# Performance work log

Hardware: AMD Instinct MI355X
Metric: run time of the kernel (lower is better)

Reference implementation:

```python
import jax, jax.numpy as jnp
import numpy as np

K_NEIGH = 12
RADIUS = 0.5


def _mlp(x, w1, b1, w2, b2):
    return jax.nn.relu(x @ w1 + b1) @ w2 + b2


def _angle(a, b):
    # atan2(||a x b||, a.b), as in PyG point-pair features
    c = jnp.cross(a, b)
    return jnp.arctan2(jnp.linalg.norm(c, axis=-1), jnp.sum(a * b, axis=-1))


def _quat_to_mat(q):
    w, x, y, z = q[:, 0], q[:, 1], q[:, 2], q[:, 3]
    m = jnp.stack([
        1 - 2 * (y * y + z * z), 2 * (x * y - z * w), 2 * (x * z + y * w),
        2 * (x * y + z * w), 1 - 2 * (x * x + z * z), 2 * (y * z - x * w),
        2 * (x * z - y * w), 2 * (y * z + x * w), 1 - 2 * (x * x + y * y),
    ], axis=-1)
    return m.reshape(-1, 3, 3)


def _lin_params(key, fan_in, fan_out):
    kw, kb = jax.random.split(key)
    s = 1.0 / np.sqrt(fan_in)
    w = jax.random.uniform(kw, (fan_in, fan_out), minval=-s, maxval=s, dtype=jnp.float32)
    b = jax.random.uniform(kb, (fan_out,), minval=-s, maxval=s, dtype=jnp.float32)
    return w, b


def setup_inputs() -> dict:
    key = jax.random.key(0)
    keys = jax.random.split(key, 8)
    points = jax.random.uniform(keys[0], (1, 128, 64, 3), dtype=jnp.float32)
    dims = [(7, 32, 16), (19, 32, 8), (24, 32, 16), (16, 32, 8), (24, 32, 16), (16, 32, 12), (27, 64, 1)]
    names = ['l1', 'g1', 'l2', 'g2', 'l3', 'g3', 'l4']
    inp = {'points': points}
    for i, (nm, (di, dh, do)) in enumerate(zip(names, dims)):
        k1, k2 = jax.random.split(keys[i + 1])
        w1, b1 = _lin_params(k1, di, dh)
        w2, b2 = _lin_params(k2, dh, do)
        inp[nm + '_w1'], inp[nm + '_b1'], inp[nm + '_w2'], inp[nm + '_b2'] = w1, b1, w2, b2
    return inp


def reference(points, l1_w1, l1_b1, l1_w2, l1_b2, g1_w1, g1_b1, g1_w2, g1_b2,
              l2_w1, l2_b1, l2_w2, l2_b2, g2_w1, g2_b1, g2_w2, g2_b2,
              l3_w1, l3_b1, l3_w2, l3_b2, g3_w1, g3_b1, g3_w2, g3_b2,
              l4_w1, l4_b1, l4_w2, l4_b2):
    B, H, W, _ = points.shape
    pos = points.reshape(-1, 3)          # [N,3]
    N = pos.shape[0]
    K = K_NEIGH
    pos_sg = jax.lax.stop_gradient(pos)  # torch detaches pos before edge features

    # --- dense radius graph: K nearest neighbors, self-padded beyond radius ---
    sq = jnp.sum(pos_sg * pos_sg, -1)
    d2 = sq[:, None] + sq[None, :] - 2.0 * (pos_sg @ pos_sg.T)  # [N,N]
    idx = jnp.arange(N)
    d2 = d2.at[idx, idx].set(jnp.inf)
    neg_d2_k, knn = jax.lax.top_k(-d2, K)
    d2_k = -neg_d2_k
    dense = jnp.where(d2_k <= RADIUS * RADIUS, knn, idx[:, None])  # [N,K]
    rows = jnp.repeat(idx, K)            # [E]
    cols = dense.reshape(-1)             # [E]

    # --- covariance of neighborhood, analytic 3x3 eig -> PCA normals ---
    nbr = pos[dense]                     # [N,K,3] (non-detached, as in torch)
    cent = jnp.mean(nbr, axis=1, keepdims=True)
    diff = nbr - cent
    cov = jnp.einsum('nki,nkj->nij', diff, diff) / K
    noise = (jax.random.uniform(jax.random.key(42), (100, 3), dtype=jnp.float32) - 0.5) * 1e-8
    cov = cov + jnp.diag(noise)          # torch.diag of (100,3) -> length-3 vector broadcast
    eig_val, eig_vec = jnp.linalg.eigh(cov)  # ascending, matches sort+gather in torch
    normals = eig_vec[:, :, 0]           # eigenvector of smallest eigenvalue
    pca_normals = normals.reshape(B, H, W, 3).transpose(0, 3, 1, 2)

    # --- edge feature stack: gather-MLP-mean-broadcast chain ---
    cart = pos_sg[cols] - pos_sg[rows]   # [E,3]
    dist = jnp.linalg.norm(cart, axis=-1)
    n_r, n_c = normals[rows], normals[cols]
    ppf = jnp.stack([dist, _angle(n_r, cart), _angle(n_c, cart), _angle(n_r, n_c)], -1)
    x = _mlp(jnp.concatenate([cart, ppf], -1), l1_w1, l1_b1, l1_w2, l1_b2)  # [E,16]

    gx = jnp.concatenate([x.reshape(N, K, -1).mean(1), normals], -1)        # [N,19]
    x_g = _mlp(gx, g1_w1, g1_b1, g1_w2, g1_b2)                              # [N,8]
    x = _mlp(jnp.concatenate([x, x_g[rows]], 1), l2_w1, l2_b1, l2_w2, l2_b2)

    x_g = _mlp(x.reshape(N, K, -1).mean(1), g2_w1, g2_b1, g2_w2, g2_b2)
    x = _mlp(jnp.concatenate([x, x_g[rows]], 1), l3_w1, l3_b1, l3_w2, l3_b2)

    x_g = _mlp(x.reshape(N, K, -1).mean(1), g3_w1, g3_b1, g3_w2, g3_b2)     # [N,12]
    quat = x_g[:, :4]
    quat = quat / (jnp.linalg.norm(quat, axis=-1) + 1e-8)[:, None]
    mat = _quat_to_mat(quat)             # [N,3,3]
    feat_g = x_g[:, 4:]
    rot_cart = jnp.einsum('eij,ej->ei', mat[rows], cart)
    x = _mlp(jnp.concatenate([x, feat_g[rows], rot_cart], 1), l4_w1, l4_b1, l4_w2, l4_b2)

    point_fea = jax.nn.softmax(x.reshape(N, K), axis=1)
    point_fea = point_fea.reshape(B, H, W, K).transpose(0, 3, 1, 2)
    return pca_normals, point_fea
```

## Files before the change

### kernel.cpp

```cpp
#include <hip/hip_runtime.h>
#include <math.h>

#define KNB 12
#define GRD 8
#define NCELL (GRD * GRD * GRD)


__device__ __forceinline__ unsigned umin32(unsigned a, unsigned b) {
    unsigned r; asm("v_min_u32 %0, %1, %2" : "=v"(r) : "v"(a), "v"(b)); return r;
}
__device__ __forceinline__ unsigned umax32(unsigned a, unsigned b) {
    unsigned r; asm("v_max_u32 %0, %1, %2" : "=v"(r) : "v"(a), "v"(b)); return r;
}

__device__ __forceinline__ float fm(float a, float b) { return __fmul_rn(a, b); }
__device__ __forceinline__ float fa(float a, float b) { return __fadd_rn(a, b); }
__device__ __forceinline__ float fs(float a, float b) { return __fsub_rn(a, b); }
__device__ __forceinline__ float fsignf(float a, float b) { return (b >= 0.0f) ? fabsf(a) : -fabsf(a); }

__device__ float slapy2_(float x, float y) {
    float xa = fabsf(x), ya = fabsf(y);
    float w = fmaxf(xa, ya), z = fminf(xa, ya);
    if (z == 0.0f) return w;
    float q = z / w;
    return fm(w, __fsqrt_rn(fa(1.0f, fm(q, q))));
}

__device__ void slartg_(float f, float g, float& c, float& s, float& r) {
    if (g == 0.0f) { c = 1.0f; s = 0.0f; r = f; }
    else if (f == 0.0f) { c = 0.0f; s = (g >= 0.0f) ? 1.0f : -1.0f; r = fabsf(g); }
    else {
        float d = __fsqrt_rn(fa(fm(f, f), fm(g, g)));
        c = fabsf(f) / d;
        r = (f >= 0.0f) ? d : -d;
        s = g / r;
    }
}

__device__ void slaev2_(float a, float b, float cc,
                        float& rt1, float& rt2, float& cs1, float& sn1) {
    float sm = fa(a, cc), df = fs(a, cc), adf = fabsf(df);
    float tb = fa(b, b), ab = fabsf(tb);
    float acmx, acmn;
    if (fabsf(a) > fabsf(cc)) { acmx = a; acmn = cc; } else { acmx = cc; acmn = a; }
    float rt;
    if (adf > ab)      { float q = ab / adf; rt = fm(adf, __fsqrt_rn(fa(1.0f, fm(q, q)))); }
    else if (adf < ab) { float q = adf / ab; rt = fm(ab,  __fsqrt_rn(fa(1.0f, fm(q, q)))); }
    else               rt = fm(ab, __fsqrt_rn(2.0f));
    int sgn1;
    if (sm < 0.0f) {
        rt1 = fm(0.5f, fs(sm, rt)); sgn1 = -1;
        rt2 = fs(fm(acmx / rt1, acmn), fm(b / rt1, b));
    } else if (sm > 0.0f) {
        rt1 = fm(0.5f, fa(sm, rt)); sgn1 = 1;
        rt2 = fs(fm(acmx / rt1, acmn), fm(b / rt1, b));
    } else { rt1 = fm(0.5f, rt); rt2 = fm(-0.5f, rt); sgn1 = 1; }
    int sgn2; float cs;
    if (df >= 0.0f) { cs = fa(df, rt); sgn2 = 1; } else { cs = fs(df, rt); sgn2 = -1; }
    float acs = fabsf(cs);
    if (acs > ab) {
        float ct = -tb / cs;
        sn1 = 1.0f / __fsqrt_rn(fa(1.0f, fm(ct, ct)));
        cs1 = fm(ct, sn1);
    } else {
        if (ab == 0.0f) { cs1 = 1.0f; sn1 = 0.0f; }
        else {
            float tn = -cs / tb;
            cs1 = 1.0f / __fsqrt_rn(fa(1.0f, fm(tn, tn)));
            sn1 = fm(tn, cs1);
        }
    }
    if (sgn1 == sgn2) { float tn = cs1; cs1 = -sn1; sn1 = tn; }
}

__device__ __forceinline__ void rot2col(float& a1, float& a2, float& a3,
                                        float& b1, float& b2, float& b3,
                                        float ct, float st) {
    float t;
    t = b1; b1 = fs(fm(ct, t), fm(st, a1)); a1 = fa(fm(st, t), fm(ct, a1));
    t = b2; b2 = fs(fm(ct, t), fm(st, a2)); a2 = fa(fm(st, t), fm(ct, a2));
    t = b3; b3 = fs(fm(ct, t), fm(st, a3)); a3 = fa(fm(st, t), fm(ct, a3));
}

#define RD(i)    ((i) == 1 ? d1 : ((i) == 2 ? d2 : d3))
#define WRD(i,v) do { float _t = (v); if ((i) == 1) d1 = _t; else if ((i) == 2) d2 = _t; else d3 = _t; } while (0)
#define RE(i)    ((i) == 1 ? e1 : e2)
#define WRE(i,v) do { float _t = (v); if ((i) == 1) e1 = _t; else e2 = _t; } while (0)
#define SWAPC(a,b) do { float _t = (a); (a) = (b); (b) = _t; } while (0)

__device__ void eig3_smallest_reg(float a00, float a10, float a20,
                                  float a11, float a21, float a22,
                                  float& v1o, float& v2o, float& v3o) {
    float z11 = 1.0f, z21 = 0.0f, z31 = 0.0f;
    float z12 = 0.0f, z22 = 1.0f, z32 = 0.0f;
    float z13 = 0.0f, z23 = 0.0f, z33 = 1.0f;
    float d1, d2, d3, e1, e2;
    float wc1 = 0.0f, wc2 = 0.0f, ws1 = 0.0f, ws2 = 0.0f;

    float tau = 0.0f, v3 = 0.0f;
    d1 = a00;
    if (a20 != 0.0f) {
        float xn = fabsf(a20);
        float beta = -fsignf(slapy2_(a10, xn), a10);
        tau = fs(beta, a10) / beta;
        float rinv = 1.0f / fs(a10, beta);
        v3 = fm(a20, rinv);
        e1 = beta;
        float w1 = fa(fm(tau, a11), fm(tau, fm(a21, v3)));
        float w2 = fa(fm(tau, a21), fm(fm(tau, v3), a22));
        float dot = fa(w1, fm(w2, v3));
        float al = fm(fm(-0.5f, tau), dot);
        w1 = fa(w1, al);
        w2 = fa(w2, fm(al, v3));
        d2 = fs(fs(a11, w1), w1);
        e2 = fs(fs(a21, fm(v3, w1)), w2);
        d3 = fs(fs(a22, fm(v3, w2)), fm(w2, v3));
    } else {
        e1 = a10; d2 = a11; e2 = a21; d3 = a22;
    }

    const float eps = 5.9604645e-8f;
    const float eps2 = 3.5527137e-15f;
    const float safmin = 1.17549435e-38f;
    int jtot = 0; const int nmaxit = 90;
    int l1 = 1;
    while (l1 <= 3) {
        if (l1 > 1) WRE(l1 - 1, 0.0f);
        int m;
        for (m = l1; m <= 2; ++m) {
            float tst = fabsf(RE(m));
            if (tst == 0.0f) break;
            if (tst <= fm(fm(__fsqrt_rn(fabsf(RD(m))), __fsqrt_rn(fabsf(RD(m + 1)))), eps)) {
                WRE(m, 0.0f); break;
            }
        }
        int l = l1, lend = m;
        l1 = m + 1;
        if (lend == l) continue;
        if (fabsf(RD(lend)) < fabsf(RD(l))) { int t = l; l = lend; lend = t; }
        if (lend > l) {
            for (;;) {
                int mq = lend;
                if (l != lend) {
                    for (mq = l; mq <= lend - 1; ++mq) {
                        float tst = fm(RE(mq), RE(mq));
                        if (tst <= fa(fm(fm(eps2, fabsf(RD(mq))), fabsf(RD(mq + 1))), safmin)) break;
                    }
                }
                if (mq < lend) WRE(mq, 0.0f);
                float p = RD(l);
                if (mq == l) { l += 1; if (l <= lend) continue; break; }
                if (mq == l + 1) {
                    float rt1, rt2, cc, ss;
                    if (l == 1) {
                        slaev2_(d1, e1, d2, rt1, rt2, cc, ss);
                        rot2col(z11, z21, z31, z12, z22, z32, cc, ss);
                        d1 = rt1; d2 = rt2; e1 = 0.0f;
                    } else {
                        slaev2_(d2, e2, d3, rt1, rt2, cc, ss);
                        rot2col(z12, z22, z32, z13, z23, z33, cc, ss);
                        d2 = rt1; d3 = rt2; e2 = 0.0f;
                    }
                    l += 2; if (l <= lend) continue; break;
                }
                if (jtot == nmaxit) break;
                jtot++;
                float g = fs(d2, p) / fm(2.0f, e1);
                float r = slapy2_(g, 1.0f);
                g = fa(fs(d3, p), e1 / fa(g, fsignf(r, g)));
                float s_ = 1.0f, c_ = 1.0f; p = 0.0f;
                {
                    float f = fm(s_, e2), b = fm(c_, e2);
                    slartg_(g, f, c_, s_, r);
                    g = fs(d3, p);
                    r = fa(fm(fs(d2, g), s_), fm(fm(2.0f, c_), b));
                    p = fm(s_, r);
                    d3 = fa(g, p);
                    g = fs(fm(c_, r), b);
                    wc2 = c_; ws2 = -s_;
                }
                {
                    float f = fm(s_, e1), b = fm(c_, e1);
                    slartg_(g, f, c_, s_, r);
                    e2 = r;
                    g = fs(d2, p);
                    r = fa(fm(fs(d1, g), s_), fm(fm(2.0f, c_), b));
                    p = fm(s_, r);
                    d2 = fa(g, p);
                    g = fs(fm(c_, r), b);
                    wc1 = c_; ws1 = -s_;
                }
                rot2col(z12, z22, z32, z13, z23, z33, wc2, ws2);
                rot2col(z11, z21, z31, z12, z22, z32, wc1, ws1);
                d1 = fs(d1, p); e1 = g;
            }
        } else {
            for (;;) {
                int mq = lend;
                if (l != lend) {
                    for (mq = l; mq >= lend + 1; --mq) {
                        float tst = fm(RE(mq - 1), RE(mq - 1));
                        if (tst <= fa(fm(fm(eps2, fabsf(RD(mq))), fabsf(RD(mq - 1))), safmin)) break;
                    }
                }
                if (mq > lend) WRE(mq - 1, 0.0f);
                float p = RD(l);
                if (mq == l) { l -= 1; if (l >= lend) continue; break; }
                if (mq == l - 1) {
                    float rt1, rt2, cc, ss;
                    if (l == 2) {
                        slaev2_(d1, e1, d2, rt1, rt2, cc, ss);
                        rot2col(z11, z21, z31, z12, z22, z32, cc, ss);
                        d1 = rt1; d2 = rt2; e1 = 0.0f;
                    } else {
                        slaev2_(d2, e2, d3, rt1, rt2, cc, ss);
                        rot2col(z12, z22, z32, z13, z23, z33, cc, ss);
                        d2 = rt1; d3 = rt2; e2 = 0.0f;
                    }
                    l -= 2; if (l >= lend) continue; break;
                }
                if (jtot == nmaxit) break;
                jtot++;
                float g = fs(d2, p) / fm(2.0f, e2);
                float r = slapy2_(g, 1.0f);
                g = fa(fs(d1, p), e2 / fa(g, fsignf(r, g)));
                float s_ = 1.0f, c_ = 1.0f; p = 0.0f;
                {
                    float f = fm(s_, e1), b = fm(c_, e1);
                    slartg_(g, f, c_, s_, r);
                    g = fs(d1, p);
                    r = fa(fm(fs(d2, g), s_), fm(fm(2.0f, c_), b));
                    p = fm(s_, r);
                    d1 = fa(g, p);
                    g = fs(fm(c_, r), b);
                    wc1 = c_; ws1 = s_;
                }
                {
                    float f = fm(s_, e2), b = fm(c_, e2);
                    slartg_(g, f, c_, s_, r);
                    e1 = r;
                    g = fs(d2, p);
                    r = fa(fm(fs(d3, g), s_), fm(fm(2.0f, c_), b));
                    p = fm(s_, r);
                    d2 = fa(g, p);
                    g = fs(fm(c_, r), b);
                    wc2 = c_; ws2 = s_;
                }
                rot2col(z11, z21, z31, z12, z22, z32, wc1, ws1);
                rot2col(z12, z22, z32, z13, z23, z33, wc2, ws2);
                d3 = fs(d3, p); e2 = g;
            }
        }
    }
    for (int ii = 2; ii <= 3; ++ii) {
        int i = ii - 1, kk = i; float p = RD(i);
        for (int j = ii; j <= 3; ++j) { float dj = RD(j); if (dj < p) { kk = j; p = dj; } }
        if (kk != i) {
            WRD(kk, RD(i)); WRD(i, p);
            if (i == 1 && kk == 2)      { SWAPC(z11, z12); SWAPC(z21, z22); SWAPC(z31, z32); }
            else if (i == 1 && kk == 3) { SWAPC(z11, z13); SWAPC(z21, z23); SWAPC(z31, z33); }
            else                        { SWAPC(z12, z13); SWAPC(z22, z23); SWAPC(z32, z33); }
        }
    }
    if (tau != 0.0f) {
        float ss, t;
        ss = fa(z21, fm(v3, z31)); t = fm(tau, ss); z21 = fs(z21, t); z31 = fs(z31, fm(t, v3));
        ss = fa(z22, fm(v3, z32)); t = fm(tau, ss); z22 = fs(z22, t); z32 = fs(z32, fm(t, v3));
        ss = fa(z23, fm(v3, z33)); t = fm(tau, ss); z23 = fs(z23, t); z33 = fs(z33, fm(t, v3));
    }
    v1o = z11; v2o = z21; v3o = z31;
}

__device__ void threefry2x32_(unsigned k0, unsigned k1, unsigned c0, unsigned c1,
                              unsigned& o0, unsigned& o1) {
    const unsigned rot[8] = {13u, 15u, 26u, 6u, 17u, 29u, 16u, 24u};
    unsigned ks[3] = {k0, k1, k0 ^ k1 ^ 0x1BD11BDAu};
    unsigned x0 = c0 + k0, x1 = c1 + k1;
    for (int blk = 0; blk < 5; ++blk) {
        const unsigned* r = &rot[(blk & 1) * 4];
        for (int i = 0; i < 4; ++i) {
            x0 += x1;
            x1 = (x1 << r[i]) | (x1 >> (32 - r[i]));
            x1 ^= x0;
        }
        x0 += ks[(blk + 1) % 3];
        x1 += ks[(blk + 2) % 3] + (unsigned)(blk + 1);
    }
    o0 = x0; o1 = x1;
}

__device__ float noise_diag_(int j) {
    unsigned m = (unsigned)(4 * j);
    unsigned o0, o1;
    threefry2x32_(0u, 42u, m, 150u + m, o0, o1);
    unsigned bits = (o0 >> 9) | 0x3f800000u;
    float u = fs(__uint_as_float(bits), 1.0f);
    return fm(fs(u, 0.5f), 1e-8f);
}

__device__ __forceinline__ float angf(float ax, float ay, float az,
                                      float bx, float by, float bz) {
    float cx = ay * bz - az * by;
    float cy = az * bx - ax * bz;
    float cz = ax * by - ay * bx;
    float cn = sqrtf(cx * cx + cy * cy + cz * cz);
    float d  = ax * bx + ay * by + az * bz;
    return atan2f(cn, d);
}


__global__ void k_prep(const float* __restrict__ pts, float4* __restrict__ pos4,
                       int* __restrict__ pcell, int* __restrict__ hist, int n) {
    int i = blockIdx.x * blockDim.x + threadIdx.x;
    if (i < n) {
        float x = pts[i * 3], y = pts[i * 3 + 1], z = pts[i * 3 + 2];
        float sq = fa(fa(fm(x, x), fm(y, y)), fm(z, z));
        pos4[i] = make_float4(x, y, z, sq);
        int cx = (int)(x * 8.0f); cx = cx < 0 ? 0 : (cx > GRD - 1 ? GRD - 1 : cx);
        int cy = (int)(y * 8.0f); cy = cy < 0 ? 0 : (cy > GRD - 1 ? GRD - 1 : cy);
        int cz = (int)(z * 8.0f); cz = cz < 0 ? 0 : (cz > GRD - 1 ? GRD - 1 : cz);
        int cid = (cz * GRD + cy) * GRD + cx;
        pcell[i] = cid;
        atomicAdd(&hist[cid], 1);
    }
}

__global__ __launch_bounds__(NCELL) void k_scan(const int* __restrict__ hist,
                                                int* __restrict__ start,
                                                int* __restrict__ cursor) {
    __shared__ int s[NCELL];
    int t = threadIdx.x;
    int v = hist[t];
    s[t] = v;
    __syncthreads();
    for (int off = 1; off < NCELL; off <<= 1) {
        int x = (t >= off) ? s[t - off] : 0;
        __syncthreads();
        s[t] += x;
        __syncthreads();
    }
    int ex = s[t] - v;
    start[t] = ex;
    cursor[t] = ex;
    if (t == NCELL - 1) start[NCELL] = s[t];
}

__global__ void k_scatter(const int* __restrict__ pcell, int* __restrict__ cursor,
                          int* __restrict__ order, int n) {
    int i = blockIdx.x * blockDim.x + threadIdx.x;
    if (i < n) {
        int slot = atomicAdd(&cursor[pcell[i]], 1);
        order[slot] = i;
    }
}

#define KEY_WORST 0xC0001FFFFFFFFFFFull
#define CBUF 128

__global__ __launch_bounds__(256) void k_knn(const float4* __restrict__ pos4,
                                             const int* __restrict__ order,
                                             const int* __restrict__ cstart,
                                             int* __restrict__ cols,
                                             float4* __restrict__ nrm4,
                                             float* __restrict__ out, int n) {
    __shared__ unsigned long long sbuf[4][CBUF];
    __shared__ int scnt[4];
    __shared__ float4 sq4[4][KNB];

    int lane = threadIdx.x & 63;
    int wv = threadIdx.x >> 6;
    int io = blockIdx.x * 4 + wv;
    if (io >= n) return;

    float4 P = pos4[io];
    int cx = (int)(P.x * 8.0f); cx = cx < 0 ? 0 : (cx > GRD - 1 ? GRD - 1 : cx);
    int cy = (int)(P.y * 8.0f); cy = cy < 0 ? 0 : (cy > GRD - 1 ? GRD - 1 : cy);
    int cz = (int)(P.z * 8.0f); cz = cz < 0 ? 0 : (cz > GRD - 1 ? GRD - 1 : cz);

    unsigned T = 0xFFFFFFFFu;
    int xlo = 0, xhi = 0, ylo = 0, yhi = 0, zlo = 0, zhi = 0;

    for (int r = 1; r < 16; ++r) {
        xlo = cx - r; if (xlo < 0) xlo = 0;
        xhi = cx + r; if (xhi > GRD - 1) xhi = GRD - 1;
        ylo = cy - r; if (ylo < 0) ylo = 0;
        yhi = cy + r; if (yhi > GRD - 1) yhi = GRD - 1;
        zlo = cz - r; if (zlo < 0) zlo = 0;
        zhi = cz + r; if (zhi > GRD - 1) zhi = GRD - 1;

        unsigned b0 = 0xFFFFFFFFu, b1 = 0xFFFFFFFFu;
        for (int zz = zlo; zz <= zhi; ++zz)
            for (int yy = ylo; yy <= yhi; ++yy) {
                int rowb = (zz * GRD + yy) * GRD;
                int jb = cstart[rowb + xlo];
                int je = cstart[rowb + xhi + 1];
                for (int t = jb + lane; t < je; t += 64) {
                    int j = order[t];
                    float4 Q = pos4[j];
                    float g = fm(P.x, Q.x);
                    g = fmaf(P.y, Q.y, g);
                    g = fmaf(P.z, Q.z, g);
                    float d2 = fs(fa(P.w, Q.w), fm(2.0f, g));
                    unsigned u = __float_as_uint(d2);
                    u = (j == io) ? 0xFFFFFFFFu : u;
                    unsigned lo = umin32(b0, u);
                    unsigned hi = umax32(b0, u);
                    b0 = lo;
                    b1 = umin32(b1, hi);
                }
            }

        {
            unsigned h0 = b0, h1 = b1;
            T = 0xFFFFFFFFu;
            for (int rr = 0; rr < KNB + 1; ++rr) {
                unsigned mn = h0;
#pragma unroll
                for (int off = 32; off >= 1; off >>= 1) {
                    unsigned o = (unsigned)__shfl_xor((int)mn, off, 64);
                    mn = umin32(mn, o);
                }
                unsigned long long bl = __ballot(h0 == mn);
                int first = __ffsll(bl) - 1;
                if (lane == first) { h0 = h1; h1 = 0xFFFFFFFFu; }
                T = mn;
            }
        }

        bool cover = (xlo == 0) && (xhi == GRD - 1) && (ylo == 0) && (yhi == GRD - 1)
                  && (zlo == 0) && (zhi == GRD - 1);
        if (cover) break;
        if (T != 0xFFFFFFFFu) {
            float gmin = 1e30f;
            if (xlo > 0)       gmin = fminf(gmin, fs(P.x, (float)xlo * 0.125f));
            if (xhi < GRD - 1) gmin = fminf(gmin, fs((float)(xhi + 1) * 0.125f, P.x));
            if (ylo > 0)       gmin = fminf(gmin, fs(P.y, (float)ylo * 0.125f));
            if (yhi < GRD - 1) gmin = fminf(gmin, fs((float)(yhi + 1) * 0.125f, P.y));
            if (zlo > 0)       gmin = fminf(gmin, fs(P.z, (float)zlo * 0.125f));
            if (zhi < GRD - 1) gmin = fminf(gmin, fs((float)(zhi + 1) * 0.125f, P.z));
            float g2 = fm(fm(gmin, gmin), 0.9995f);
            if (__uint_as_float(T) <= g2) break;
        }
    }

    if (lane == 0) scnt[wv] = 0;
    __builtin_amdgcn_wave_barrier();
    for (int zz = zlo; zz <= zhi; ++zz)
        for (int yy = ylo; yy <= yhi; ++yy) {
            int rowb = (zz * GRD + yy) * GRD;
            int jb = cstart[rowb + xlo];
            int je = cstart[rowb + xhi + 1];
            for (int t = jb + lane; t < je; t += 64) {
                int j = order[t];
                float4 Q = pos4[j];
                float g = fm(P.x, Q.x);
                g = fmaf(P.y, Q.y, g);
                g = fmaf(P.z, Q.z, g);
                float d2 = fs(fa(P.w, Q.w), fm(2.0f, g));
                unsigned u = __float_as_uint(d2);
                bool c = (u <= T) && (j != io);
                unsigned long long bl = __ballot(c);
                if (bl) {
                    int leader = __ffsll(bl) - 1;
                    int base = 0;
                    if (lane == leader)
                        base = atomicAdd(&scnt[wv], (int)__popcll(bl));
                    base = __shfl(base, leader, 64);
                    if (c) {
                        int pos = base + (int)__popcll(bl & ((1ull << lane) - 1ull));
                        unsigned us = u ^ (unsigned)(((int)u >> 31) | 0x80000000);
                        unsigned long long kb = (((unsigned long long)us << 13) | (unsigned)j)
                                                | 0xC000000000000000ull;
                        if (pos < CBUF) sbuf[wv][pos] = kb;
                    }
                }
            }
        }
    __builtin_amdgcn_wave_barrier();
    int cnt = scnt[wv];
    if (cnt > CBUF) cnt = CBUF;

    double k0 = __longlong_as_double((long long)KEY_WORST);
    double k1 = __longlong_as_double((long long)KEY_WORST);
    if (lane < cnt) k0 = __longlong_as_double((long long)sbuf[wv][lane]);
    if (lane + 64 < cnt) k1 = __longlong_as_double((long long)sbuf[wv][lane + 64]);
    double mykey = __longlong_as_double((long long)KEY_WORST);
    for (int rr = 0; rr < KNB; ++rr) {
        double mx = fmax(k0, k1);
#pragma unroll
        for (int off = 32; off >= 1; off >>= 1)
            mx = fmax(mx, __shfl_xor(mx, off, 64));
        if (k0 == mx) k0 = __longlong_as_double((long long)KEY_WORST);
        else if (k1 == mx) k1 = __longlong_as_double((long long)KEY_WORST);
        if (lane == rr) mykey = mx;
    }
    if (lane < KNB) {
        unsigned long long bits = (unsigned long long)__double_as_longlong(mykey);
        unsigned j = (unsigned)(bits & 0x1FFFu);
        unsigned u = (unsigned)((bits >> 13) & 0xFFFFFFFFull);
        unsigned ob = (u & 0x80000000u) ? (u ^ 0x80000000u) : ~u;
        float d2 = __uint_as_float(ob);
        int cv = (d2 <= 0.25f) ? (int)j : io;
        cols[io * KNB + lane] = cv;
        float4 qp = pos4[cv];
        sq4[wv][lane] = make_float4(qp.x, qp.y, qp.z, 0.0f);
    }
    __builtin_amdgcn_wave_barrier();

    if (lane == 0) {
        float qx[KNB], qy[KNB], qz[KNB];
#pragma unroll
        for (int k = 0; k < KNB; ++k) {
            float4 q = sq4[wv][k];
            qx[k] = q.x; qy[k] = q.y; qz[k] = q.z;
        }
        float sx = qx[0], sy = qy[0], sz = qz[0];
#pragma unroll
        for (int k = 1; k < KNB; ++k) { sx = fa(sx, qx[k]); sy = fa(sy, qy[k]); sz = fa(sz, qz[k]); }
        float mx = sx / 12.0f, my = sy / 12.0f, mz = sz / 12.0f;
        float c00 = 0, c10 = 0, c20 = 0, c11 = 0, c21 = 0, c22 = 0;
#pragma unroll
        for (int k = 0; k < KNB; ++k) {
            float dx = fs(qx[k], mx), dy = fs(qy[k], my), dz = fs(qz[k], mz);
            c00 = fa(c00, fm(dx, dx));
            c10 = fa(c10, fm(dy, dx));
            c20 = fa(c20, fm(dz, dx));
            c11 = fa(c11, fm(dy, dy));
            c21 = fa(c21, fm(dz, dy));
            c22 = fa(c22, fm(dz, dz));
        }
        c00 = c00 / 12.0f; c10 = c10 / 12.0f; c20 = c20 / 12.0f;
        c11 = c11 / 12.0f; c21 = c21 / 12.0f; c22 = c22 / 12.0f;
        float v0 = noise_diag_(0), v1 = noise_diag_(1), v2 = noise_diag_(2);
        float a00 = fa(c00, v0), a10 = fa(c10, v0), a20 = fa(c20, v0);
        float a11 = fa(c11, v1), a21 = fa(c21, v1), a22 = fa(c22, v2);
        float e1, e2, e3;
        eig3_smallest_reg(a00, a10, a20, a11, a21, a22, e1, e2, e3);
        nrm4[io] = make_float4(e1, e2, e3, 0.0f);
        out[io]         = e1;
        out[n + io]     = e2;
        out[2 * n + io] = e3;
    }
}


struct WPtrs { const float* p[28]; };

template <int NI, int NH, int NO>
__device__ __forceinline__ void mlp_half(const float* __restrict__ w1, const float* __restrict__ b1,
                                         const float* __restrict__ w2, const float* __restrict__ b2,
                                         const float* in, float* out, int hf) {
#pragma unroll
    for (int o = 0; o < NO; ++o) out[o] = hf ? 0.0f : b2[o];
    const int HH = NH / 2;
    int h0 = hf * HH;
    for (int hi = 0; hi < HH; ++hi) {
        int h = h0 + hi;
        float hh = b1[h];
#pragma unroll
        for (int ii = 0; ii < NI; ++ii) hh = fmaf(in[ii], w1[ii * NH + h], hh);
        hh = fmaxf(hh, 0.0f);
#pragma unroll
        for (int o = 0; o < NO; ++o) out[o] = fmaf(hh, w2[h * NO + o], out[o]);
    }
}

template <int NI, int NO>
__device__ __forceinline__ void gmlp_part(const float* __restrict__ w1, const float* __restrict__ b1,
                                          const float* __restrict__ w2, const float* __restrict__ b2,
                                          const float* in, float* pout, int q) {
#pragma unroll
    for (int o = 0; o < NO; ++o) pout[o] = (q == 0) ? b2[o] : 0.0f;
    {
        float hh = b1[q];
#pragma unroll
        for (int ii = 0; ii < NI; ++ii) hh = fmaf(in[ii], w1[ii * 32 + q], hh);
        hh = fmaxf(hh, 0.0f);
#pragma unroll
        for (int o = 0; o < NO; ++o) pout[o] = fmaf(hh, w2[q * NO + o], pout[o]);
    }
    if (q < 8) {
        int h = 24 + q;
        float hh = b1[h];
#pragma unroll
        for (int ii = 0; ii < NI; ++ii) hh = fmaf(in[ii], w1[ii * 32 + h], hh);
        hh = fmaxf(hh, 0.0f);
#pragma unroll
        for (int o = 0; o < NO; ++o) pout[o] = fmaf(hh, w2[h * NO + o], pout[o]);
    }
}

#define SCR(pp, qq, oo) s_scr[((pp) * 24 + (qq)) * 17 + (oo)]
#define SM(pp, oo)      s_m[(pp) * 17 + (oo)]
#define GFV(pp, oo)     s_g[(pp) * 13 + (oo)]
#define SLG(pp, kk)     s_log[(pp) * 13 + (kk)]

__global__ __launch_bounds__(384) void k_mlp(const float4* __restrict__ pos4,
                                             const int* __restrict__ cols,
                                             const float4* __restrict__ nrm4,
                                             WPtrs wp, float* __restrict__ out, int n) {
    __shared__ float s_scr[16 * 24 * 17];
    __shared__ float s_m[16 * 17];
    __shared__ float s_g[16 * 13];
    __shared__ float s_log[16 * 13];
    __shared__ float s_red[16 * 2];

    int t = threadIdx.x;
    int tm = t % 192;
    int p = tm / 12, k = tm - p * 12;
    int hf = __builtin_amdgcn_readfirstlane(t / 192);
    int q = hf * 12 + k;
    int nn = blockIdx.x * 16 + p;
    bool act = (nn < n);

    float cx = 0, cy = 0, cz = 0, nrx = 0, nry = 0, nrz = 0;
    float xr[16];

    if (act) {
        int col = cols[nn * 12 + k];
        float4 P = pos4[nn], Q = pos4[col];
        cx = Q.x - P.x; cy = Q.y - P.y; cz = Q.z - P.z;
        float dist = sqrtf(cx * cx + cy * cy + cz * cz);
        float4 NR = nrm4[nn], NC = nrm4[col];
        nrx = NR.x; nry = NR.y; nrz = NR.z;
        float a1 = angf(nrx, nry, nrz, cx, cy, cz);
        float a2 = angf(NC.x, NC.y, NC.z, cx, cy, cz);
        float a3 = angf(nrx, nry, nrz, NC.x, NC.y, NC.z);
        float in7[7] = {cx, cy, cz, dist, a1, a2, a3};
        float px[16];
        mlp_half<7, 32, 16>(wp.p[0], wp.p[1], wp.p[2], wp.p[3], in7, px, hf);
#pragma unroll
        for (int o = 0; o < 16; ++o) SCR(p, q, o) = px[o];
    }
    __syncthreads();
    if (act) {
#pragma unroll
        for (int o = 0; o < 16; ++o) xr[o] = SCR(p, k, o) + SCR(p, 12 + k, o);
    }
    __syncthreads();

    if (act && q < 16) {
        float s = 0.0f;
        for (int kk = 0; kk < 12; ++kk) s += SCR(p, kk, q) + SCR(p, 12 + kk, q);
        SM(p, q) = s / 12.0f;
    }
    __syncthreads();
    if (act) {
        float gin[19];
#pragma unroll
        for (int ii = 0; ii < 16; ++ii) gin[ii] = SM(p, ii);
        gin[16] = nrx; gin[17] = nry; gin[18] = nrz;
        float pg[8];
        gmlp_part<19, 8>(wp.p[4], wp.p[5], wp.p[6], wp.p[7], gin, pg, q);
#pragma unroll
        for (int o = 0; o < 8; ++o) SCR(p, q, o) = pg[o];
    }
    __syncthreads();
    if (act && q < 8) {
        float s = 0.0f;
        for (int j = 0; j < 24; ++j) s += SCR(p, j, q);
        GFV(p, q) = s;
    }
    __syncthreads();

    if (act) {
        float in24[24];
#pragma unroll
        for (int o = 0; o < 16; ++o) in24[o] = xr[o];
#pragma unroll
        for (int o = 0; o < 8; ++o) in24[16 + o] = GFV(p, o);
        float px[16];
        mlp_half<24, 32, 16>(wp.p[8], wp.p[9], wp.p[10], wp.p[11], in24, px, hf);
#pragma unroll
        for (int o = 0; o < 16; ++o) SCR(p, q, o) = px[o];
    }
    __syncthreads();
    if (act) {
#pragma unroll
        for (int o = 0; o < 16; ++o) xr[o] = SCR(p, k, o) + SCR(p, 12 + k, o);
    }
    __syncthreads();

    if (act && q < 16) {
        float s = 0.0f;
        for (int kk = 0; kk < 12; ++kk) s += SCR(p, kk, q) + SCR(p, 12 + kk, q);
        SM(p, q) = s / 12.0f;
    }
    __syncthreads();
    if (act) {
        float gin[16];
#pragma unroll
        for (int ii = 0; ii < 16; ++ii) gin[ii] = SM(p, ii);
        float pg[8];
        gmlp_part<16, 8>(wp.p[12], wp.p[13], wp.p[14], wp.p[15], gin, pg, q);
#pragma unroll
        for (int o = 0; o < 8; ++o) SCR(p, q, o) = pg[o];
    }
    __syncthreads();
    if (act && q < 8) {
        float s = 0.0f;
        for (int j = 0; j < 24; ++j) s += SCR(p, j, q);
        GFV(p, q) = s;
    }
    __syncthreads();

    if (act) {
        float in24[24];
#pragma unroll
        for (int o = 0; o < 16; ++o) in24[o] = xr[o];
#pragma unroll
        for (int o = 0; o < 8; ++o) in24[16 + o] = GFV(p, o);
        float px[16];
        mlp_half<24, 32, 16>(wp.p[16], wp.p[17], wp.p[18], wp.p[19], in24, px, hf);
#pragma unroll
        for (int o = 0; o < 16; ++o) SCR(p, q, o) = px[o];
    }
    __syncthreads();
    if (act) {
#pragma unroll
        for (int o = 0; o < 16; ++o) xr[o] = SCR(p, k, o) + SCR(p, 12 + k, o);
    }
    __syncthreads();

    if (act && q < 16) {
        float s = 0.0f;
        for (int kk = 0; kk < 12; ++kk) s += SCR(p, kk, q) + SCR(p, 12 + kk, q);
        SM(p, q) = s / 12.0f;
    }
    __syncthreads();
    if (act) {
        float gin[16];
#pragma unroll
        for (int ii = 0; ii < 16; ++ii) gin[ii] = SM(p, ii);
        float pg[12];
        gmlp_part<16, 12>(wp.p[20], wp.p[21], wp.p[22], wp.p[23], gin, pg, q);
#pragma unroll
        for (int o = 0; o < 12; ++o) SCR(p, q, o) = pg[o];
    }
    __syncthreads();
    if (act && q < 12) {
        float s = 0.0f;
        for (int j = 0; j < 24; ++j) s += SCR(p, j, q);
        GFV(p, q) = s;
    }
    __syncthreads();

    if (act) {
        float g0 = GFV(p, 0), g1v = GFV(p, 1), g2v = GFV(p, 2), g3v = GFV(p, 3);
        float qn = sqrtf(g0 * g0 + g1v * g1v + g2v * g2v + g3v * g3v) + 1e-8f;
        float qw = g0 / qn, qxx = g1v / qn, qyy = g2v / qn, qzz = g3v / qn;
        float m0 = 1.0f - 2.0f * (qyy * qyy + qzz * qzz);
        float m1 = 2.0f * (qxx * qyy - qzz * qw);
        float m2 = 2.0f * (qxx * qzz + qyy * qw);
        float m3 = 2.0f * (qxx * qyy + qzz * qw);
        float m4 = 1.0f - 2.0f * (qxx * qxx + qzz * qzz);
        float m5 = 2.0f * (qyy * qzz - qxx * qw);
        float m6 = 2.0f * (qxx * qzz - qyy * qw);
        float m7 = 2.0f * (qyy * qzz + qxx * qw);
        float m8 = 1.0f - 2.0f * (qxx * qxx + qyy * qyy);
        float r0 = m0 * cx + m1 * cy + m2 * cz;
        float r1 = m3 * cx + m4 * cy + m5 * cz;
        float r2 = m6 * cx + m7 * cy + m8 * cz;
        float in27[27];
#pragma unroll
        for (int o = 0; o < 16; ++o) in27[o] = xr[o];
#pragma unroll
        for (int o = 0; o < 8; ++o) in27[16 + o] = GFV(p, 4 + o);
        in27[24] = r0; in27[25] = r1; in27[26] = r2;
        float plg[1];
        mlp_half<27, 64, 1>(wp.p[24], wp.p[25], wp.p[26], wp.p[27], in27, plg, hf);
        SCR(p, q, 0) = plg[0];
    }
    __syncthreads();
    if (act && hf == 0) SLG(p, k) = SCR(p, k, 0) + SCR(p, 12 + k, 0);
    __syncthreads();

    if (act && q == 0) {
        float mx = SLG(p, 0);
        for (int kk = 1; kk < 12; ++kk) mx = fmaxf(mx, SLG(p, kk));
        float se = 0;
        for (int kk = 0; kk < 12; ++kk) se += expf(SLG(p, kk) - mx);
        s_red[p * 2] = mx; s_red[p * 2 + 1] = se;
    }
    __syncthreads();
    if (act && hf == 0) {
        float v = expf(SLG(p, k) - s_red[p * 2]) / s_red[p * 2 + 1];
        out[3 * n + k * n + nn] = v;
    }
}


extern "C" void kernel_launch(void* const* d_in, const int* in_sizes, int n_in,
                              void* d_out, int out_size, void* d_ws, size_t ws_size,
                              hipStream_t stream) {
    const float* pts = (const float*)d_in[0];
    int n = in_sizes[0] / 3;

    char* ws = (char*)d_ws;
    float4* pos4  = (float4*)ws;
    int*    cols  = (int*)(ws + (size_t)n * 16);
    float4* nrm4  = (float4*)(ws + (size_t)n * 64);
    int*    pcell = (int*)(ws + (size_t)n * 80);
    int*    order = (int*)(ws + (size_t)n * 84);
    int*    hist  = (int*)(ws + (size_t)n * 88);
    int*    start = hist + NCELL;
    int*    cursor = start + NCELL + 1;
    float*  out = (float*)d_out;

    WPtrs wp;
    for (int a = 0; a < 28; ++a) wp.p[a] = (const float*)d_in[a + 1];

    hipMemsetAsync(hist, 0, NCELL * sizeof(int), stream);
    k_prep<<<(n + 255) / 256, 256, 0, stream>>>(pts, pos4, pcell, hist, n);
    k_scan<<<1, NCELL, 0, stream>>>(hist, start, cursor);
    k_scatter<<<(n + 255) / 256, 256, 0, stream>>>(pcell, cursor, order, n);
    k_knn<<<(n + 3) / 4, 256, 0, stream>>>(pos4, order, start, cols, nrm4, out, n);
    k_mlp<<<(n + 15) / 16, 384, 0, stream>>>(pos4, cols, nrm4, wp, out, n);
}
```

Measured before the change: 217.7 us.

## Fuse grid build into one block and parallelize per-point PCA across waves

The memset and the prep, scan and scatter kernels are merged into one single-block kernel that builds the cell histogram, scan and order array in shared memory. This removes three launches and a memset for a small N of 8192. In k_knn, the per-point covariance and eigen step now runs on 4 lanes of wave 0 after a block barrier, one lane per point, rather than lane 0 of each wave. A single block doing the whole build serializes it on one CU, and the added __syncthreads makes waves wait for each other.

Measured after the change: 223.7 us. +2.7%, slower.

```diff
diff --git a/kernel.cpp b/kernel.cpp
--- a/kernel.cpp
+++ b/kernel.cpp
@@ -308,11 +308,18 @@
     return atan2f(cn, d);
 }
 
-
-__global__ void k_prep(const float* __restrict__ pts, float4* __restrict__ pos4,
-                       int* __restrict__ pcell, int* __restrict__ hist, int n) {
-    int i = blockIdx.x * blockDim.x + threadIdx.x;
-    if (i < n) {
+__global__ __launch_bounds__(1024) void k_build(const float* __restrict__ pts,
+                                                float4* __restrict__ pos4,
+                                                int* __restrict__ order,
+                                                int* __restrict__ start, int n) {
+    __shared__ int sh[NCELL];
+    __shared__ int scur[NCELL];
+    int t = threadIdx.x;
+
+    for (int c = t; c < NCELL; c += 1024) sh[c] = 0;
+    __syncthreads();
+
+    for (int i = t; i < n; i += 1024) {
         float x = pts[i * 3], y = pts[i * 3 + 1], z = pts[i * 3 + 2];
         float sq = fa(fa(fm(x, x), fm(y, y)), fm(z, z));
         pos4[i] = make_float4(x, y, z, sq);
@@ -320,36 +327,34 @@
         int cy = (int)(y * 8.0f); cy = cy < 0 ? 0 : (cy > GRD - 1 ? GRD - 1 : cy);
         int cz = (int)(z * 8.0f); cz = cz < 0 ? 0 : (cz > GRD - 1 ? GRD - 1 : cz);
         int cid = (cz * GRD + cy) * GRD + cx;
-        pcell[i] = cid;
-        atomicAdd(&hist[cid], 1);
-    }
-}
-
-__global__ __launch_bounds__(NCELL) void k_scan(const int* __restrict__ hist,
-                                                int* __restrict__ start,
-                                                int* __restrict__ cursor) {
-    __shared__ int s[NCELL];
-    int t = threadIdx.x;
-    int v = hist[t];
-    s[t] = v;
-    __syncthreads();
+        atomicAdd(&sh[cid], 1);
+    }
+    __syncthreads();
+
+    int v = 0;
+    if (t < NCELL) v = sh[t];
     for (int off = 1; off < NCELL; off <<= 1) {
-        int x = (t >= off) ? s[t - off] : 0;
+        int x = 0;
+        if (t < NCELL && t >= off) x = sh[t - off];
         __syncthreads();
-        s[t] += x;
+        if (t < NCELL) sh[t] += x;
         __syncthreads();
     }
-    int ex = s[t] - v;
-    start[t] = ex;
-    cursor[t] = ex;
-    if (t == NCELL - 1) start[NCELL] = s[t];
-}
-
-__global__ void k_scatter(const int* __restrict__ pcell, int* __restrict__ cursor,
-                          int* __restrict__ order, int n) {
-    int i = blockIdx.x * blockDim.x + threadIdx.x;
-    if (i < n) {
-        int slot = atomicAdd(&cursor[pcell[i]], 1);
+    if (t < NCELL) {
+        int ex = sh[t] - v;
+        start[t] = ex;
+        scur[t] = ex;
+        if (t == NCELL - 1) start[NCELL] = sh[t];
+    }
+    __syncthreads();
+
+    for (int i = t; i < n; i += 1024) {
+        float4 P = pos4[i];
+        int cx = (int)(P.x * 8.0f); cx = cx < 0 ? 0 : (cx > GRD - 1 ? GRD - 1 : cx);
+        int cy = (int)(P.y * 8.0f); cy = cy < 0 ? 0 : (cy > GRD - 1 ? GRD - 1 : cy);
+        int cz = (int)(P.z * 8.0f); cz = cz < 0 ? 0 : (cz > GRD - 1 ? GRD - 1 : cz);
+        int cid = (cz * GRD + cy) * GRD + cx;
+        int slot = atomicAdd(&scur[cid], 1);
         order[slot] = i;
     }
 }
@@ -370,25 +375,82 @@
     int lane = threadIdx.x & 63;
     int wv = threadIdx.x >> 6;
     int io = blockIdx.x * 4 + wv;
-    if (io >= n) return;
-
-    float4 P = pos4[io];
-    int cx = (int)(P.x * 8.0f); cx = cx < 0 ? 0 : (cx > GRD - 1 ? GRD - 1 : cx);
-    int cy = (int)(P.y * 8.0f); cy = cy < 0 ? 0 : (cy > GRD - 1 ? GRD - 1 : cy);
-    int cz = (int)(P.z * 8.0f); cz = cz < 0 ? 0 : (cz > GRD - 1 ? GRD - 1 : cz);
-
-    unsigned T = 0xFFFFFFFFu;
-    int xlo = 0, xhi = 0, ylo = 0, yhi = 0, zlo = 0, zhi = 0;
-
-    for (int r = 1; r < 16; ++r) {
-        xlo = cx - r; if (xlo < 0) xlo = 0;
-        xhi = cx + r; if (xhi > GRD - 1) xhi = GRD - 1;
-        ylo = cy - r; if (ylo < 0) ylo = 0;
-        yhi = cy + r; if (yhi > GRD - 1) yhi = GRD - 1;
-        zlo = cz - r; if (zlo < 0) zlo = 0;
-        zhi = cz + r; if (zhi > GRD - 1) zhi = GRD - 1;
-
-        unsigned b0 = 0xFFFFFFFFu, b1 = 0xFFFFFFFFu;
+    bool wact = (io < n);
+
+    if (wact) {
+        float4 P = pos4[io];
+        int cx = (int)(P.x * 8.0f); cx = cx < 0 ? 0 : (cx > GRD - 1 ? GRD - 1 : cx);
+        int cy = (int)(P.y * 8.0f); cy = cy < 0 ? 0 : (cy > GRD - 1 ? GRD - 1 : cy);
+        int cz = (int)(P.z * 8.0f); cz = cz < 0 ? 0 : (cz > GRD - 1 ? GRD - 1 : cz);
+
+        unsigned T = 0xFFFFFFFFu;
+        int xlo = 0, xhi = 0, ylo = 0, yhi = 0, zlo = 0, zhi = 0;
+
+        for (int r = 1; r < 16; ++r) {
+            xlo = cx - r; if (xlo < 0) xlo = 0;
+            xhi = cx + r; if (xhi > GRD - 1) xhi = GRD - 1;
+            ylo = cy - r; if (ylo < 0) ylo = 0;
+            yhi = cy + r; if (yhi > GRD - 1) yhi = GRD - 1;
+            zlo = cz - r; if (zlo < 0) zlo = 0;
+            zhi = cz + r; if (zhi > GRD - 1) zhi = GRD - 1;
+
+            unsigned b0 = 0xFFFFFFFFu, b1 = 0xFFFFFFFFu;
+            for (int zz = zlo; zz <= zhi; ++zz)
+                for (int yy = ylo; yy <= yhi; ++yy) {
+                    int rowb = (zz * GRD + yy) * GRD;
+                    int jb = cstart[rowb + xlo];
+                    int je = cstart[rowb + xhi + 1];
+                    for (int t = jb + lane; t < je; t += 64) {
+                        int j = order[t];
+                        float4 Q = pos4[j];
+                        float g = fm(P.x, Q.x);
+                        g = fmaf(P.y, Q.y, g);
+                        g = fmaf(P.z, Q.z, g);
+                        float d2 = fs(fa(P.w, Q.w), fm(2.0f, g));
+                        unsigned u = __float_as_uint(d2);
+                        u = (j == io) ? 0xFFFFFFFFu : u;
+                        unsigned lo = umin32(b0, u);
+                        unsigned hi = umax32(b0, u);
+                        b0 = lo;
+                        b1 = umin32(b1, hi);
+                    }
+                }
+
+            {
+                unsigned h0 = b0, h1 = b1;
+                T = 0xFFFFFFFFu;
+                for (int rr = 0; rr < KNB + 1; ++rr) {
+                    unsigned mn = h0;
+#pragma unroll
+                    for (int off = 32; off >= 1; off >>= 1) {
+                        unsigned o = (unsigned)__shfl_xor((int)mn, off, 64);
+                        mn = umin32(mn, o);
+                    }
+                    unsigned long long bl = __ballot(h0 == mn);
+                    int first = __ffsll(bl) - 1;
+                    if (lane == first) { h0 = h1; h1 = 0xFFFFFFFFu; }
+                    T = mn;
+                }
+            }
+
+            bool cover = (xlo == 0) && (xhi == GRD - 1) && (ylo == 0) && (yhi == GRD - 1)
+                      && (zlo == 0) && (zhi == GRD - 1);
+            if (cover) break;
+            if (T != 0xFFFFFFFFu) {
+                float gmin = 1e30f;
+                if (xlo > 0)       gmin = fminf(gmin, fs(P.x, (float)xlo * 0.125f));
+                if (xhi < GRD - 1) gmin = fminf(gmin, fs((float)(xhi + 1) * 0.125f, P.x));
+                if (ylo > 0)       gmin = fminf(gmin, fs(P.y, (float)ylo * 0.125f));
+                if (yhi < GRD - 1) gmin = fminf(gmin, fs((float)(yhi + 1) * 0.125f, P.y));
+                if (zlo > 0)       gmin = fminf(gmin, fs(P.z, (float)zlo * 0.125f));
+                if (zhi < GRD - 1) gmin = fminf(gmin, fs((float)(zhi + 1) * 0.125f, P.z));
+                float g2 = fm(fm(gmin, gmin), 0.9995f);
+                if (__uint_as_float(T) <= g2) break;
+            }
+        }
+
+        if (lane == 0) scnt[wv] = 0;
+        __builtin_amdgcn_wave_barrier();
         for (int zz = zlo; zz <= zhi; ++zz)
             for (int yy = ylo; yy <= yhi; ++yy) {
                 int rowb = (zz * GRD + yy) * GRD;
@@ -402,144 +464,92 @@
                     g = fmaf(P.z, Q.z, g);
                     float d2 = fs(fa(P.w, Q.w), fm(2.0f, g));
                     unsigned u = __float_as_uint(d2);
-                    u = (j == io) ? 0xFFFFFFFFu : u;
-                    unsigned lo = umin32(b0, u);
-                    unsigned hi = umax32(b0, u);
-                    b0 = lo;
-                    b1 = umin32(b1, hi);
+                    bool c = (u <= T) && (j != io);
+                    unsigned long long bl = __ballot(c);
+                    if (bl) {
+                        int leader = __ffsll(bl) - 1;
+                        int base = 0;
+                        if (lane == leader)
+                            base = atomicAdd(&scnt[wv], (int)__popcll(bl));
+                        base = __shfl(base, leader, 64);
+                        if (c) {
+                            int pos = base + (int)__popcll(bl & ((1ull << lane) - 1ull));
+                            unsigned us = u ^ (unsigned)(((int)u >> 31) | 0x80000000);
+                            unsigned long long kb = (((unsigned long long)us << 13) | (unsigned)j)
+                                                    | 0xC000000000000000ull;
+                            if (pos < CBUF) sbuf[wv][pos] = kb;
+                        }
+                    }
                 }
             }
-
-        {
-            unsigned h0 = b0, h1 = b1;
-            T = 0xFFFFFFFFu;
-            for (int rr = 0; rr < KNB + 1; ++rr) {
-                unsigned mn = h0;
-#pragma unroll
-                for (int off = 32; off >= 1; off >>= 1) {
-                    unsigned o = (unsigned)__shfl_xor((int)mn, off, 64);
-                    mn = umin32(mn, o);
-                }
-                unsigned long long bl = __ballot(h0 == mn);
-                int first = __ffsll(bl) - 1;
-                if (lane == first) { h0 = h1; h1 = 0xFFFFFFFFu; }
-                T = mn;
+        __builtin_amdgcn_wave_barrier();
+        int cnt = scnt[wv];
+        if (cnt > CBUF) cnt = CBUF;
+
+        double k0 = __longlong_as_double((long long)KEY_WORST);
+        double k1 = __longlong_as_double((long long)KEY_WORST);
+        if (lane < cnt) k0 = __longlong_as_double((long long)sbuf[wv][lane]);
+        if (lane + 64 < cnt) k1 = __longlong_as_double((long long)sbuf[wv][lane + 64]);
+        double mykey = __longlong_as_double((long long)KEY_WORST);
+        for (int rr = 0; rr < KNB; ++rr) {
+            double mx = fmax(k0, k1);
+#pragma unroll
+            for (int off = 32; off >= 1; off >>= 1)
+                mx = fmax(mx, __shfl_xor(mx, off, 64));
+            if (k0 == mx) k0 = __longlong_as_double((long long)KEY_WORST);
+            else if (k1 == mx) k1 = __longlong_as_double((long long)KEY_WORST);
+            if (lane == rr) mykey = mx;
+        }
+        if (lane < KNB) {
+            unsigned long long bits = (unsigned long long)__double_as_longlong(mykey);
+            unsigned j = (unsigned)(bits & 0x1FFFu);
+            unsigned u = (unsigned)((bits >> 13) & 0xFFFFFFFFull);
+            unsigned ob = (u & 0x80000000u) ? (u ^ 0x80000000u) : ~u;
+            float d2 = __uint_as_float(ob);
+            int cv = (d2 <= 0.25f) ? (int)j : io;
+            cols[io * KNB + lane] = cv;
+            float4 qp = pos4[cv];
+            sq4[wv][lane] = make_float4(qp.x, qp.y, qp.z, 0.0f);
+        }
+    }
+    __syncthreads();
+
+    if (wv == 0 && lane < 4) {
+        int pp = blockIdx.x * 4 + lane;
+        if (pp < n) {
+            float qx[KNB], qy[KNB], qz[KNB];
+#pragma unroll
+            for (int k = 0; k < KNB; ++k) {
+                float4 q = sq4[lane][k];
+                qx[k] = q.x; qy[k] = q.y; qz[k] = q.z;
             }
+            float sx = qx[0], sy = qy[0], sz = qz[0];
+#pragma unroll
+            for (int k = 1; k < KNB; ++k) { sx = fa(sx, qx[k]); sy = fa(sy, qy[k]); sz = fa(sz, qz[k]); }
+            float mx = sx / 12.0f, my = sy / 12.0f, mz = sz / 12.0f;
+            float c00 = 0, c10 = 0, c20 = 0, c11 = 0, c21 = 0, c22 = 0;
+#pragma unroll
+            for (int k = 0; k < KNB; ++k) {
+                float dx = fs(qx[k], mx), dy = fs(qy[k], my), dz = fs(qz[k], mz);
+                c00 = fa(c00, fm(dx, dx));
+                c10 = fa(c10, fm(dy, dx));
+                c20 = fa(c20, fm(dz, dx));
+                c11 = fa(c11, fm(dy, dy));
+                c21 = fa(c21, fm(dz, dy));
+                c22 = fa(c22, fm(dz, dz));
+            }
+            c00 = c00 / 12.0f; c10 = c10 / 12.0f; c20 = c20 / 12.0f;
+            c11 = c11 / 12.0f; c21 = c21 / 12.0f; c22 = c22 / 12.0f;
+            float v0 = noise_diag_(0), v1 = noise_diag_(1), v2 = noise_diag_(2);
+            float a00 = fa(c00, v0), a10 = fa(c10, v0), a20 = fa(c20, v0);
+            float a11 = fa(c11, v1), a21 = fa(c21, v1), a22 = fa(c22, v2);
+            float e1, e2, e3;
+            eig3_smallest_reg(a00, a10, a20, a11, a21, a22, e1, e2, e3);
+            nrm4[pp] = make_float4(e1, e2, e3, 0.0f);
+            out[pp]         = e1;
+            out[n + pp]     = e2;
+            out[2 * n + pp] = e3;
         }
-
-        bool cover = (xlo == 0) && (xhi == GRD - 1) && (ylo == 0) && (yhi == GRD - 1)
-                  && (zlo == 0) && (zhi == GRD - 1);
-        if (cover) break;
-        if (T != 0xFFFFFFFFu) {
-            float gmin = 1e30f;
-            if (xlo > 0)       gmin = fminf(gmin, fs(P.x, (float)xlo * 0.125f));
-            if (xhi < GRD - 1) gmin = fminf(gmin, fs((float)(xhi + 1) * 0.125f, P.x));
-            if (ylo > 0)       gmin = fminf(gmin, fs(P.y, (float)ylo * 0.125f));
-            if (yhi < GRD - 1) gmin = fminf(gmin, fs((float)(yhi + 1) * 0.125f, P.y));
-            if (zlo > 0)       gmin = fminf(gmin, fs(P.z, (float)zlo * 0.125f));
-            if (zhi < GRD - 1) gmin = fminf(gmin, fs((float)(zhi + 1) * 0.125f, P.z));
-            float g2 = fm(fm(gmin, gmin), 0.9995f);
-            if (__uint_as_float(T) <= g2) break;
-        }
-    }
-
-    if (lane == 0) scnt[wv] = 0;
-    __builtin_amdgcn_wave_barrier();
-    for (int zz = zlo; zz <= zhi; ++zz)
-        for (int yy = ylo; yy <= yhi; ++yy) {
-            int rowb = (zz * GRD + yy) * GRD;
-            int jb = cstart[rowb + xlo];
-            int je = cstart[rowb + xhi + 1];
-            for (int t = jb + lane; t < je; t += 64) {
-                int j = order[t];
-                float4 Q = pos4[j];
-                float g = fm(P.x, Q.x);
-                g = fmaf(P.y, Q.y, g);
-                g = fmaf(P.z, Q.z, g);
-                float d2 = fs(fa(P.w, Q.w), fm(2.0f, g));
-                unsigned u = __float_as_uint(d2);
-                bool c = (u <= T) && (j != io);
-                unsigned long long bl = __ballot(c);
-                if (bl) {
-                    int leader = __ffsll(bl) - 1;
-                    int base = 0;
-                    if (lane == leader)
-                        base = atomicAdd(&scnt[wv], (int)__popcll(bl));
-                    base = __shfl(base, leader, 64);
-                    if (c) {
-                        int pos = base + (int)__popcll(bl & ((1ull << lane) - 1ull));
-                        unsigned us = u ^ (unsigned)(((int)u >> 31) | 0x80000000);
-                        unsigned long long kb = (((unsigned long long)us << 13) | (unsigned)j)
-                                                | 0xC000000000000000ull;
-                        if (pos < CBUF) sbuf[wv][pos] = kb;
-                    }
-                }
-            }
-        }
-    __builtin_amdgcn_wave_barrier();
-    int cnt = scnt[wv];
-    if (cnt > CBUF) cnt = CBUF;
-
-    double k0 = __longlong_as_double((long long)KEY_WORST);
-    double k1 = __longlong_as_double((long long)KEY_WORST);
-    if (lane < cnt) k0 = __longlong_as_double((long long)sbuf[wv][lane]);
-    if (lane + 64 < cnt) k1 = __longlong_as_double((long long)sbuf[wv][lane + 64]);
-    double mykey = __longlong_as_double((long long)KEY_WORST);
-    for (int rr = 0; rr < KNB; ++rr) {
-        double mx = fmax(k0, k1);
-#pragma unroll
-        for (int off = 32; off >= 1; off >>= 1)
-            mx = fmax(mx, __shfl_xor(mx, off, 64));
-        if (k0 == mx) k0 = __longlong_as_double((long long)KEY_WORST);
-        else if (k1 == mx) k1 = __longlong_as_double((long long)KEY_WORST);
-        if (lane == rr) mykey = mx;
-    }
-    if (lane < KNB) {
-        unsigned long long bits = (unsigned long long)__double_as_longlong(mykey);
-        unsigned j = (unsigned)(bits & 0x1FFFu);
-        unsigned u = (unsigned)((bits >> 13) & 0xFFFFFFFFull);
-        unsigned ob = (u & 0x80000000u) ? (u ^ 0x80000000u) : ~u;
-        float d2 = __uint_as_float(ob);
-        int cv = (d2 <= 0.25f) ? (int)j : io;
-        cols[io * KNB + lane] = cv;
-        float4 qp = pos4[cv];
-        sq4[wv][lane] = make_float4(qp.x, qp.y, qp.z, 0.0f);
-    }
-    __builtin_amdgcn_wave_barrier();
-
-    if (lane == 0) {
-        float qx[KNB], qy[KNB], qz[KNB];
-#pragma unroll
-        for (int k = 0; k < KNB; ++k) {
-            float4 q = sq4[wv][k];
-            qx[k] = q.x; qy[k] = q.y; qz[k] = q.z;
-        }
-        float sx = qx[0], sy = qy[0], sz = qz[0];
-#pragma unroll
-        for (int k = 1; k < KNB; ++k) { sx = fa(sx, qx[k]); sy = fa(sy, qy[k]); sz = fa(sz, qz[k]); }
-        float mx = sx / 12.0f, my = sy / 12.0f, mz = sz / 12.0f;
-        float c00 = 0, c10 = 0, c20 = 0, c11 = 0, c21 = 0, c22 = 0;
-#pragma unroll
-        for (int k = 0; k < KNB; ++k) {
-            float dx = fs(qx[k], mx), dy = fs(qy[k], my), dz = fs(qz[k], mz);
-            c00 = fa(c00, fm(dx, dx));
-            c10 = fa(c10, fm(dy, dx));
-            c20 = fa(c20, fm(dz, dx));
-            c11 = fa(c11, fm(dy, dy));
-            c21 = fa(c21, fm(dz, dy));
-            c22 = fa(c22, fm(dz, dz));
-        }
-        c00 = c00 / 12.0f; c10 = c10 / 12.0f; c20 = c20 / 12.0f;
-        c11 = c11 / 12.0f; c21 = c21 / 12.0f; c22 = c22 / 12.0f;
-        float v0 = noise_diag_(0), v1 = noise_diag_(1), v2 = noise_diag_(2);
-        float a00 = fa(c00, v0), a10 = fa(c10, v0), a20 = fa(c20, v0);
-        float a11 = fa(c11, v1), a21 = fa(c21, v1), a22 = fa(c22, v2);
-        float e1, e2, e3;
-        eig3_smallest_reg(a00, a10, a20, a11, a21, a22, e1, e2, e3);
-        nrm4[io] = make_float4(e1, e2, e3, 0.0f);
-        out[io]         = e1;
-        out[n + io]     = e2;
-        out[2 * n + io] = e3;
     }
 }
 
@@ -800,20 +810,14 @@
     float4* pos4  = (float4*)ws;
     int*    cols  = (int*)(ws + (size_t)n * 16);
     float4* nrm4  = (float4*)(ws + (size_t)n * 64);
-    int*    pcell = (int*)(ws + (size_t)n * 80);
-    int*    order = (int*)(ws + (size_t)n * 84);
-    int*    hist  = (int*)(ws + (size_t)n * 88);
-    int*    start = hist + NCELL;
-    int*    cursor = start + NCELL + 1;
+    int*    order = (int*)(ws + (size_t)n * 80);
+    int*    start = (int*)(ws + (size_t)n * 84);
     float*  out = (float*)d_out;
 
     WPtrs wp;
     for (int a = 0; a < 28; ++a) wp.p[a] = (const float*)d_in[a + 1];
 
-    hipMemsetAsync(hist, 0, NCELL * sizeof(int), stream);
-    k_prep<<<(n + 255) / 256, 256, 0, stream>>>(pts, pos4, pcell, hist, n);
-    k_scan<<<1, NCELL, 0, stream>>>(hist, start, cursor);
-    k_scatter<<<(n + 255) / 256, 256, 0, stream>>>(pcell, cursor, order, n);
+    k_build<<<1, 1024, 0, stream>>>(pts, pos4, order, start, n);
     k_knn<<<(n + 3) / 4, 256, 0, stream>>>(pos4, order, start, cols, nrm4, out, n);
     k_mlp<<<(n + 15) / 16, 384, 0, stream>>>(pos4, cols, nrm4, wp, out, n);
 }
```
